# Kernel optimization log

Measured on AMD Instinct MI355X. Metric: run time of the kernel, lower is better.

Reference implementation:

```python
import jax, jax.numpy as jnp
import numpy as np

N_MELS = 80
FORMANT_START, FORMANT_END = 10, 50
W_L1, W_DELTA, W_DELTA2, W_SC, W_BAND, FORMANT_W = 1.0, 0.5, 0.25, 0.5, 1.0, 2.0
EPS = 1e-8


def _masked_mean(x, mask):
    # mask broadcasts to x's shape; count = sum of the broadcast mask
    n = jnp.maximum(jnp.sum(jnp.broadcast_to(mask, x.shape)), 1.0)
    return jnp.sum(x * mask) / n


def setup_inputs() -> dict:
    key = jax.random.key(0)
    k1, k2, k3 = jax.random.split(key, 3)
    B, T, D = 64, 4000, N_MELS
    pred_mel = jax.random.normal(k1, (B, T, D), dtype=jnp.float32)
    target_mel = jax.random.normal(k2, (B, T, D), dtype=jnp.float32)
    lengths = jax.random.randint(k3, (B,), T // 2, T + 1)
    mel_mask = (jnp.arange(T)[None, :] < lengths[:, None]).astype(jnp.float32)
    band_weights = jnp.ones((D,), dtype=jnp.float32).at[FORMANT_START:FORMANT_END].set(FORMANT_W)
    return {"pred_mel": pred_mel, "target_mel": target_mel, "mel_mask": mel_mask,
            "band_weights": band_weights}


def reference(pred_mel, target_mel, mel_mask, band_weights):
    mask3 = mel_mask[:, :, None]                      # (B,T,1)

    l1 = jnp.abs(pred_mel - target_mel)               # (B,T,D)
    l1_loss = _masked_mean(l1, mask3)

    # 1st-order deltas
    dp = pred_mel[:, 1:] - pred_mel[:, :-1]
    dt = target_mel[:, 1:] - target_mel[:, :-1]
    dmask = (mel_mask[:, 1:] * mel_mask[:, :-1])[:, :, None]
    delta_loss = _masked_mean(jnp.abs(dp - dt), dmask)

    # 2nd-order deltas
    d2p = dp[:, 1:] - dp[:, :-1]
    d2t = dt[:, 1:] - dt[:, :-1]
    d2mask = (mel_mask[:, 2:] * mel_mask[:, 1:-1] * mel_mask[:, :-2])[:, :, None]
    delta2_loss = _masked_mean(jnp.abs(d2p - d2t), d2mask)

    # spectral convergence
    diff = (pred_mel - target_mel) * mask3
    tgt_m = target_mel * mask3
    n = jnp.maximum(jnp.sum(jnp.broadcast_to(mask3, pred_mel.shape)), 1.0)
    sc_num = jnp.sqrt(jnp.sum(diff * diff) / n)
    sc_den = jnp.maximum(jnp.sqrt(jnp.sum(tgt_m * tgt_m) / n), EPS)
    sc_loss = sc_num / sc_den

    # band-weighted L1
    w = band_weights[None, None, :]
    band_loss = _masked_mean(l1 * w, mask3) / jnp.mean(band_weights)

    # energy (per-frame mean over mel bins)
    e_l1 = jnp.abs(pred_mel.mean(axis=-1) - target_mel.mean(axis=-1))  # (B,T)
    energy_loss = _masked_mean(e_l1, mel_mask)

    return (W_L1 * l1_loss + W_DELTA * delta_loss + W_DELTA2 * delta2_loss
            + W_SC * sc_loss + W_BAND * band_loss + 0.5 * energy_loss)
```

## Files before the change

### kernel.cpp

```cpp
#include <hip/hip_runtime.h>
#include <math.h>

#define D_MELS 80
#define T_DIM  4000
#define NQ     10


__global__ __launch_bounds__(256) void mel_loss_main(
    const float* __restrict__ pred, const float* __restrict__ tgt,
    const float* __restrict__ mask, const float* __restrict__ w,
    float* __restrict__ ws, int BT)
{
    int r = blockIdx.x * blockDim.x + threadIdx.x;

    float v_l1 = 0.f, v_band = 0.f, v_diff2 = 0.f, v_tgt2 = 0.f, v_energy = 0.f;
    float v_m = 0.f, v_d = 0.f, v_dm = 0.f, v_d2 = 0.f, v_d2m = 0.f;

    if (r < BT) {
        int t = r % T_DIM;
        bool has1 = (t >= 1);
        bool has2 = (t >= 2);

        const float* p0 = pred + (size_t)r * D_MELS;
        const float* q0 = tgt  + (size_t)r * D_MELS;
        const float* p1 = has1 ? p0 - D_MELS     : p0;
        const float* q1 = has1 ? q0 - D_MELS     : q0;
        const float* p2 = has2 ? p0 - 2 * D_MELS : p0;
        const float* q2 = has2 ? q0 - 2 * D_MELS : q0;

        float mt  = mask[r];
        float mt1 = has1 ? mask[r - 1] : 0.f;
        float mt2 = has2 ? mask[r - 2] : 0.f;

        float l1r = 0.f, bandr = 0.f, sqr = 0.f, t2r = 0.f, er = 0.f;
        float dr = 0.f, d2r = 0.f;

        #pragma unroll
        for (int j = 0; j < D_MELS / 4; ++j) {
            float4 p  = ((const float4*)p0)[j];
            float4 q  = ((const float4*)q0)[j];
            float4 pa = ((const float4*)p1)[j];
            float4 qa = ((const float4*)q1)[j];
            float4 pb = ((const float4*)p2)[j];
            float4 qb = ((const float4*)q2)[j];
            float4 wv = ((const float4*)w)[j];

            float e0 = p.x - q.x, e1 = p.y - q.y, e2 = p.z - q.z, e3 = p.w - q.w;
            float f0 = pa.x - qa.x, f1 = pa.y - qa.y, f2 = pa.z - qa.z, f3 = pa.w - qa.w;
            float g0 = pb.x - qb.x, g1 = pb.y - qb.y, g2 = pb.z - qb.z, g3 = pb.w - qb.w;

            float a0 = fabsf(e0), a1 = fabsf(e1), a2 = fabsf(e2), a3 = fabsf(e3);
            l1r   += a0 + a1 + a2 + a3;
            bandr += a0 * wv.x + a1 * wv.y + a2 * wv.z + a3 * wv.w;
            sqr   += e0 * e0 + e1 * e1 + e2 * e2 + e3 * e3;
            t2r   += q.x * q.x + q.y * q.y + q.z * q.z + q.w * q.w;
            er    += e0 + e1 + e2 + e3;
            dr  += fabsf(e0 - f0) + fabsf(e1 - f1) + fabsf(e2 - f2) + fabsf(e3 - f3);
            d2r += fabsf(e0 - 2.f * f0 + g0) + fabsf(e1 - 2.f * f1 + g1)
                 + fabsf(e2 - 2.f * f2 + g2) + fabsf(e3 - 2.f * f3 + g3);
        }

        float dmv  = mt * mt1;
        float d2mv = mt * mt1 * mt2;

        v_l1     = l1r * mt;
        v_band   = bandr * mt;
        v_diff2  = sqr * mt;
        v_tgt2   = t2r * mt;
        v_energy = fabsf(er) * mt;
        v_m      = mt;
        v_d      = dr * dmv;
        v_dm     = dmv;
        v_d2     = d2r * d2mv;
        v_d2m    = d2mv;
    }

    float vals[NQ] = {v_l1, v_band, v_diff2, v_tgt2, v_energy,
                      v_m, v_d, v_dm, v_d2, v_d2m};
    #pragma unroll
    for (int q = 0; q < NQ; ++q) {
        float v = vals[q];
        #pragma unroll
        for (int off = 32; off > 0; off >>= 1)
            v += __shfl_down(v, off, 64);
        vals[q] = v;
    }

    __shared__ float red[4][NQ];
    int wave = threadIdx.x >> 6;
    int lane = threadIdx.x & 63;
    if (lane == 0) {
        #pragma unroll
        for (int q = 0; q < NQ; ++q) red[wave][q] = vals[q];
    }
    __syncthreads();
    if (threadIdx.x < NQ) {
        float s = red[0][threadIdx.x] + red[1][threadIdx.x]
                + red[2][threadIdx.x] + red[3][threadIdx.x];
        atomicAdd(&ws[threadIdx.x], s);
    }
}

__global__ void mel_loss_finalize(const float* __restrict__ ws,
                                  const float* __restrict__ w,
                                  float* __restrict__ out)
{
    if (blockIdx.x == 0 && threadIdx.x == 0) {
        float l1s = ws[0], bands = ws[1], diff2 = ws[2], tgt2 = ws[3];
        float energys = ws[4], ms = ws[5], ds = ws[6], dms = ws[7];
        float d2s = ws[8], d2ms = ws[9];

        float wsum = 0.f;
        for (int d = 0; d < D_MELS; ++d) wsum += w[d];
        float wmean = wsum / (float)D_MELS;

        float n1  = fmaxf(ms  * (float)D_MELS, 1.f);
        float nd  = fmaxf(dms * (float)D_MELS, 1.f);
        float nd2 = fmaxf(d2ms * (float)D_MELS, 1.f);

        float l1_loss     = l1s / n1;
        float delta_loss  = ds / nd;
        float delta2_loss = d2s / nd2;
        float sc_num = sqrtf(diff2 / n1);
        float sc_den = fmaxf(sqrtf(tgt2 / n1), 1e-8f);
        float sc_loss = sc_num / sc_den;
        float band_loss = (bands / n1) / wmean;
        float energy_loss = (energys / (float)D_MELS) / fmaxf(ms, 1.f);

        out[0] = 1.0f * l1_loss + 0.5f * delta_loss + 0.25f * delta2_loss
               + 0.5f * sc_loss + 1.0f * band_loss + 0.5f * energy_loss;
    }
}

extern "C" void kernel_launch(void* const* d_in, const int* in_sizes, int n_in,
                              void* d_out, int out_size, void* d_ws, size_t ws_size,
                              hipStream_t stream) {
    const float* pred = (const float*)d_in[0];
    const float* tgt  = (const float*)d_in[1];
    const float* mask = (const float*)d_in[2];
    const float* w    = (const float*)d_in[3];
    int BT = in_sizes[2];
    float* ws = (float*)d_ws;

    hipMemsetAsync(ws, 0, NQ * sizeof(float), stream);

    int block = 256;
    int grid = (BT + block - 1) / block;
    mel_loss_main<<<grid, block, 0, stream>>>(pred, tgt, mask, w, ws, BT);
    mel_loss_finalize<<<1, 64, 0, stream>>>(ws, w, (float*)d_out);
}
```

Baseline: 234.3 us.

## Split each frame across 20 threads for coalesced loads with grid-stride loop

Instead of one thread processing a whole 80-bin frame with strided float4 loads, each frame is handled by 20 threads that each load one float4, so a wave reads contiguous memory. A persistent grid of 800 blocks loops over frames, and the per-frame energy sum is rebuilt through shared memory with two barriers per iteration. This is meant to fix uncoalesced per-thread row access. The cost is extra synchronization and 5-wave blocks.

Result: faster. 198.9 us (-15.1%).

```diff
diff --git a/kernel.cpp b/kernel.cpp
--- a/kernel.cpp
+++ b/kernel.cpp
@@ -4,75 +4,96 @@
 #define D_MELS 80
 #define T_DIM  4000
 #define NQ     10
+#define RPB    16
+#define NTHR   (RPB * 20)
+#define NWAVES (NTHR / 64)
+#define NBLK   800
 
 
-__global__ __launch_bounds__(256) void mel_loss_main(
+__global__ __launch_bounds__(NTHR) void mel_loss_main(
     const float* __restrict__ pred, const float* __restrict__ tgt,
     const float* __restrict__ mask, const float* __restrict__ w,
     float* __restrict__ ws, int BT)
 {
-    int r = blockIdx.x * blockDim.x + threadIdx.x;
+    const int tid = threadIdx.x;
+    const int g   = tid % 20;
+    const int rl  = tid / 20;
+
+    const float4* p4 = (const float4*)pred;
+    const float4* q4 = (const float4*)tgt;
+    const float4  wv = ((const float4*)w)[g];
 
     float v_l1 = 0.f, v_band = 0.f, v_diff2 = 0.f, v_tgt2 = 0.f, v_energy = 0.f;
     float v_m = 0.f, v_d = 0.f, v_dm = 0.f, v_d2 = 0.f, v_d2m = 0.f;
 
-    if (r < BT) {
-        int t = r % T_DIM;
-        bool has1 = (t >= 1);
-        bool has2 = (t >= 2);
+    __shared__ float esum[NTHR];
+    __shared__ float red[NWAVES][NQ];
 
-        const float* p0 = pred + (size_t)r * D_MELS;
-        const float* q0 = tgt  + (size_t)r * D_MELS;
-        const float* p1 = has1 ? p0 - D_MELS     : p0;
-        const float* q1 = has1 ? q0 - D_MELS     : q0;
-        const float* p2 = has2 ? p0 - 2 * D_MELS : p0;
-        const float* q2 = has2 ? q0 - 2 * D_MELS : q0;
+    for (int base = blockIdx.x * RPB; base < BT; base += gridDim.x * RPB) {
+        int r = base + rl;
+        float my_e = 0.f;
+        if (r < BT) {
+            int t = r % T_DIM;
+            bool has1 = (t >= 1);
+            bool has2 = (t >= 2);
 
-        float mt  = mask[r];
-        float mt1 = has1 ? mask[r - 1] : 0.f;
-        float mt2 = has2 ? mask[r - 2] : 0.f;
+            int i0 = r * 20 + g;
+            int i1 = has1 ? i0 - 20 : i0;
+            int i2 = has2 ? i0 - 40 : i0;
 
-        float l1r = 0.f, bandr = 0.f, sqr = 0.f, t2r = 0.f, er = 0.f;
-        float dr = 0.f, d2r = 0.f;
+            float4 p  = p4[i0];
+            float4 q  = q4[i0];
+            float4 pa = p4[i1];
+            float4 qa = q4[i1];
+            float4 pb = p4[i2];
+            float4 qb = q4[i2];
 
-        #pragma unroll
-        for (int j = 0; j < D_MELS / 4; ++j) {
-            float4 p  = ((const float4*)p0)[j];
-            float4 q  = ((const float4*)q0)[j];
-            float4 pa = ((const float4*)p1)[j];
-            float4 qa = ((const float4*)q1)[j];
-            float4 pb = ((const float4*)p2)[j];
-            float4 qb = ((const float4*)q2)[j];
-            float4 wv = ((const float4*)w)[j];
+            float mt  = mask[r];
+            float mt1 = has1 ? mask[r - 1] : 0.f;
+            float mt2 = has2 ? mask[r - 2] : 0.f;
 
             float e0 = p.x - q.x, e1 = p.y - q.y, e2 = p.z - q.z, e3 = p.w - q.w;
             float f0 = pa.x - qa.x, f1 = pa.y - qa.y, f2 = pa.z - qa.z, f3 = pa.w - qa.w;
             float g0 = pb.x - qb.x, g1 = pb.y - qb.y, g2 = pb.z - qb.z, g3 = pb.w - qb.w;
 
             float a0 = fabsf(e0), a1 = fabsf(e1), a2 = fabsf(e2), a3 = fabsf(e3);
-            l1r   += a0 + a1 + a2 + a3;
-            bandr += a0 * wv.x + a1 * wv.y + a2 * wv.z + a3 * wv.w;
-            sqr   += e0 * e0 + e1 * e1 + e2 * e2 + e3 * e3;
-            t2r   += q.x * q.x + q.y * q.y + q.z * q.z + q.w * q.w;
-            er    += e0 + e1 + e2 + e3;
-            dr  += fabsf(e0 - f0) + fabsf(e1 - f1) + fabsf(e2 - f2) + fabsf(e3 - f3);
-            d2r += fabsf(e0 - 2.f * f0 + g0) + fabsf(e1 - 2.f * f1 + g1)
-                 + fabsf(e2 - 2.f * f2 + g2) + fabsf(e3 - 2.f * f3 + g3);
+
+            float l1r   = a0 + a1 + a2 + a3;
+            float bandr = a0 * wv.x + a1 * wv.y + a2 * wv.z + a3 * wv.w;
+            float sqr   = e0 * e0 + e1 * e1 + e2 * e2 + e3 * e3;
+            float t2r   = q.x * q.x + q.y * q.y + q.z * q.z + q.w * q.w;
+            float dr  = fabsf(e0 - f0) + fabsf(e1 - f1) + fabsf(e2 - f2) + fabsf(e3 - f3);
+            float d2r = fabsf(e0 - 2.f * f0 + g0) + fabsf(e1 - 2.f * f1 + g1)
+                      + fabsf(e2 - 2.f * f2 + g2) + fabsf(e3 - 2.f * f3 + g3);
+
+            float dmv  = mt * mt1;
+            float d2mv = mt * mt1 * mt2;
+
+            v_l1    += l1r * mt;
+            v_band  += bandr * mt;
+            v_diff2 += sqr * mt;
+            v_tgt2  += t2r * mt;
+            v_d     += dr * dmv;
+            v_d2    += d2r * d2mv;
+            if (g == 0) {
+                v_m   += mt;
+                v_dm  += dmv;
+                v_d2m += d2mv;
+            }
+            my_e = e0 + e1 + e2 + e3;
         }
-
-        float dmv  = mt * mt1;
-        float d2mv = mt * mt1 * mt2;
-
-        v_l1     = l1r * mt;
-        v_band   = bandr * mt;
-        v_diff2  = sqr * mt;
-        v_tgt2   = t2r * mt;
-        v_energy = fabsf(er) * mt;
-        v_m      = mt;
-        v_d      = dr * dmv;
-        v_dm     = dmv;
-        v_d2     = d2r * d2mv;
-        v_d2m    = d2mv;
+        esum[tid] = my_e;
+        __syncthreads();
+        if (tid < RPB) {
+            int rr = base + tid;
+            if (rr < BT) {
+                float s = 0.f;
+                #pragma unroll
+                for (int k = 0; k < 20; ++k) s += esum[tid * 20 + k];
+                v_energy += fabsf(s) * mask[rr];
+            }
+        }
+        __syncthreads();
     }
 
     float vals[NQ] = {v_l1, v_band, v_diff2, v_tgt2, v_energy,
@@ -86,18 +107,18 @@
         vals[q] = v;
     }
 
-    __shared__ float red[4][NQ];
-    int wave = threadIdx.x >> 6;
-    int lane = threadIdx.x & 63;
+    int wave = tid >> 6;
+    int lane = tid & 63;
     if (lane == 0) {
         #pragma unroll
         for (int q = 0; q < NQ; ++q) red[wave][q] = vals[q];
     }
     __syncthreads();
-    if (threadIdx.x < NQ) {
-        float s = red[0][threadIdx.x] + red[1][threadIdx.x]
-                + red[2][threadIdx.x] + red[3][threadIdx.x];
-        atomicAdd(&ws[threadIdx.x], s);
+    if (tid < NQ) {
+        float s = 0.f;
+        #pragma unroll
+        for (int wv2 = 0; wv2 < NWAVES; ++wv2) s += red[wv2][tid];
+        atomicAdd(&ws[tid], s);
     }
 }
 
@@ -144,8 +165,6 @@
 
     hipMemsetAsync(ws, 0, NQ * sizeof(float), stream);
 
-    int block = 256;
-    int grid = (BT + block - 1) / block;
-    mel_loss_main<<<grid, block, 0, stream>>>(pred, tgt, mask, w, ws, BT);
+    mel_loss_main<<<NBLK, NTHR, 0, stream>>>(pred, tgt, mask, w, ws, BT);
     mel_loss_finalize<<<1, 64, 0, stream>>>(ws, w, (float*)d_out);
 }
```
